# Kernel optimization log

Measured on AMD Instinct MI355X. Metric: run time of the kernel, lower is better.

The kernel has to match this reference:

```python
import jax, jax.numpy as jnp
import numpy as np

N_NODES = 100000
N_EDGES = 3200000
D = 256


def setup_inputs() -> dict:
    key = jax.random.key(0)
    ks = jax.random.split(key, 8)
    ego_embeddings = jax.random.normal(ks[0], (N_NODES, D), dtype=jnp.float32) * 0.1
    edge_vals = jax.random.uniform(ks[1], (N_EDGES,), dtype=jnp.float32) / 32.0  # ~normalized adjacency
    W1 = jax.random.normal(ks[2], (D, D), dtype=jnp.float32) * (1.0 / np.sqrt(D))
    b1 = jnp.zeros((D,), dtype=jnp.float32)
    W2 = jax.random.normal(ks[3], (D, D), dtype=jnp.float32) * (1.0 / np.sqrt(D))
    b2 = jnp.zeros((D,), dtype=jnp.float32)
    edge_rows = jax.random.randint(ks[4], (N_EDGES,), 0, N_NODES, dtype=jnp.int32)
    edge_cols = jax.random.randint(ks[5], (N_EDGES,), 0, N_NODES, dtype=jnp.int32)
    return {"ego_embeddings": ego_embeddings, "edge_vals": edge_vals,
            "W1": W1, "b1": b1, "W2": W2, "b2": b2,
            "edge_rows": edge_rows, "edge_cols": edge_cols}


def reference(ego_embeddings, edge_vals, W1, b1, W2, b2, edge_rows, edge_cols):
    # SpMM: side = A_in @ ego  (A_in in COO: rows, cols, vals)
    n = ego_embeddings.shape[0]
    gathered = ego_embeddings[edge_cols] * edge_vals[:, None]      # [E, D]
    side = jax.ops.segment_sum(gathered, edge_rows, num_segments=n)  # [N, D]
    # bi-interaction aggregator
    sum_emb = jax.nn.leaky_relu((ego_embeddings + side) @ W1.T + b1, negative_slope=0.01)
    bi_emb = jax.nn.leaky_relu((ego_embeddings * side) @ W2.T + b2, negative_slope=0.01)
    # dropout p=0.0 -> identity
    return sum_emb + bi_emb
```

## Files before the change

### kernel.cpp

```cpp
#include <hip/hip_runtime.h>
#include <hip/hip_fp16.h>
#include <stdint.h>

#define D 256
#define CHSH 13

typedef __attribute__((ext_vector_type(8))) short short8;
typedef __attribute__((ext_vector_type(4))) float floatx4;

__device__ __forceinline__ ushort f2bf(float f) {
    union { float f; uint32_t u; } v; v.f = f;
    uint32_t u = v.u;
    u += 0x7fffu + ((u >> 16) & 1u);
    return (ushort)(u >> 16);
}
__device__ __forceinline__ float bf2f(ushort h) {
    union { uint32_t u; float f; } v; v.u = ((uint32_t)h) << 16;
    return v.f;
}


__global__ void k_hist(const int* __restrict__ er, const int* __restrict__ ec,
                       int* __restrict__ bp, int E, int NCH) {
    int e = blockIdx.x * 256 + threadIdx.x;
    if (e >= E) return;
    atomicAdd(&bp[er[e] * NCH + (ec[e] >> CHSH)], 1);
}

__global__ void k_red(const int* __restrict__ bp, int* __restrict__ part, int nb) {
    __shared__ int s[256];
    int t = threadIdx.x;
    int base = blockIdx.x * 1024 + t * 4;
    int v = 0;
#pragma unroll
    for (int j = 0; j < 4; ++j) if (base + j < nb) v += bp[base + j];
    s[t] = v; __syncthreads();
    for (int off = 128; off; off >>= 1) {
        if (t < off) s[t] += s[t + off];
        __syncthreads();
    }
    if (t == 0) part[blockIdx.x] = s[0];
}

__global__ __launch_bounds__(1024) void k_scanpart(int* __restrict__ part, int np) {
    __shared__ int s[1024];
    int t = threadIdx.x;
    int p0 = (2 * t < np) ? part[2 * t] : 0;
    int p1 = (2 * t + 1 < np) ? part[2 * t + 1] : 0;
    int v = p0 + p1;
    s[t] = v; __syncthreads();
    for (int off = 1; off < 1024; off <<= 1) {
        int x = (t >= off) ? s[t - off] : 0;
        __syncthreads();
        s[t] += x;
        __syncthreads();
    }
    int excl = s[t] - v;
    if (2 * t < np) part[2 * t] = excl;
    if (2 * t + 1 < np) part[2 * t + 1] = excl + p0;
}

__global__ void k_scan3(int* __restrict__ bp, const int* __restrict__ part, int nb) {
    __shared__ int s[256];
    int t = threadIdx.x;
    int base = blockIdx.x * 1024 + t * 4;
    int d0 = 0, d1 = 0, d2 = 0, d3 = 0;
    if (base     < nb) d0 = bp[base];
    if (base + 1 < nb) d1 = bp[base + 1];
    if (base + 2 < nb) d2 = bp[base + 2];
    if (base + 3 < nb) d3 = bp[base + 3];
    int sum = d0 + d1 + d2 + d3;
    s[t] = sum; __syncthreads();
    for (int off = 1; off < 256; off <<= 1) {
        int x = (t >= off) ? s[t - off] : 0;
        __syncthreads();
        s[t] += x;
        __syncthreads();
    }
    int run = part[blockIdx.x] + s[t] - sum;
    if (base     < nb) bp[base]     = run; run += d0;
    if (base + 1 < nb) bp[base + 1] = run; run += d1;
    if (base + 2 < nb) bp[base + 2] = run; run += d2;
    if (base + 3 < nb) bp[base + 3] = run;
}

__global__ void k_scatter(const int* __restrict__ er, const int* __restrict__ ec,
                          const float* __restrict__ ev, int* __restrict__ bp,
                          uint32_t* __restrict__ csr, int E, int NCH) {
    int e = blockIdx.x * 256 + threadIdx.x;
    if (e >= E) return;
    int col = ec[e];
    int p = atomicAdd(&bp[er[e] * NCH + (col >> CHSH)], 1);
    ushort hb = __half_as_ushort(__float2half_rn(ev[e]));
    csr[p] = ((uint32_t)col << 15) | (uint32_t)hb;
}

__global__ void k_cvt(const float4* __restrict__ ego, ushort4* __restrict__ ego_bf,
                      const float4* __restrict__ W1, const float4* __restrict__ W2,
                      ushort4* __restrict__ W1b, ushort4* __restrict__ W2b, int n4) {
    int i = blockIdx.x * 256 + threadIdx.x;
    const float4* src;
    ushort4* dst;
    if (i < n4) { src = ego + i; dst = ego_bf + i; }
    else {
        int j = i - n4;
        if (j >= 32768) return;
        int k = j & 16383;
        src = ((j < 16384) ? W1 : W2) + k;
        dst = ((j < 16384) ? W1b : W2b) + k;
    }
    float4 f = *src;
    ushort4 u;
    u.x = f2bf(f.x); u.y = f2bf(f.y); u.z = f2bf(f.z); u.w = f2bf(f.w);
    *dst = u;
}

__global__ void k_spmm(const ushort* __restrict__ ego_bf, const int* __restrict__ bp,
                       const uint32_t* __restrict__ csr,
                       ushort* __restrict__ X1, ushort* __restrict__ X2, int n, int NCH) {
    int gtid = blockIdx.x * 256 + threadIdx.x;
    int node = gtid >> 6;
    int lane = gtid & 63;
    if (node >= n) return;
    int beg = (node == 0) ? 0 : bp[node * NCH - 1];
    int end = bp[(node + 1) * NCH - 1];
    int d0 = lane * 4;
    float a0 = 0.f, a1 = 0.f, a2 = 0.f, a3 = 0.f;
    int e = beg;
    for (; e + 8 <= end; e += 8) {
        uint32_t w[8];
#pragma unroll
        for (int j = 0; j < 8; ++j) w[j] = csr[e + j];
        ushort4 u[8];
#pragma unroll
        for (int j = 0; j < 8; ++j)
            u[j] = *(const ushort4*)(ego_bf + (size_t)(w[j] >> 15) * D + d0);
#pragma unroll
        for (int j = 0; j < 8; ++j) {
            float v = __half2float(__ushort_as_half((ushort)(w[j] & 0x7fff)));
            a0 += v * bf2f(u[j].x);
            a1 += v * bf2f(u[j].y);
            a2 += v * bf2f(u[j].z);
            a3 += v * bf2f(u[j].w);
        }
    }
    for (; e < end; ++e) {
        uint32_t w = csr[e];
        float v = __half2float(__ushort_as_half((ushort)(w & 0x7fff)));
        ushort4 u = *(const ushort4*)(ego_bf + (size_t)(w >> 15) * D + d0);
        a0 += v * bf2f(u.x);
        a1 += v * bf2f(u.y);
        a2 += v * bf2f(u.z);
        a3 += v * bf2f(u.w);
    }
    ushort4 eg = *(const ushort4*)(ego_bf + (size_t)node * D + d0);
    float e0 = bf2f(eg.x), e1 = bf2f(eg.y), e2 = bf2f(eg.z), e3 = bf2f(eg.w);
    ushort4 o1, o2;
    o1.x = f2bf(e0 + a0); o2.x = f2bf(e0 * a0);
    o1.y = f2bf(e1 + a1); o2.y = f2bf(e1 * a1);
    o1.z = f2bf(e2 + a2); o2.z = f2bf(e2 * a2);
    o1.w = f2bf(e3 + a3); o2.w = f2bf(e3 * a3);
    *(ushort4*)(X1 + (size_t)node * D + d0) = o1;
    *(ushort4*)(X2 + (size_t)node * D + d0) = o2;
}

__global__ __launch_bounds__(256) void k_gemm(
        const ushort* __restrict__ X1, const ushort* __restrict__ X2,
        const ushort* __restrict__ W1b, const ushort* __restrict__ W2b,
        const float* __restrict__ b1, const float* __restrict__ b2,
        float* __restrict__ out, int n) {
    int lane = threadIdx.x & 63;
    int w = threadIdx.x >> 6;
    int l16 = lane & 15, quad = lane >> 4;
    int row0 = blockIdx.x * 64;
    int colw = w * 64;

    floatx4 acc1[4][4], acc2[4][4];
#pragma unroll
    for (int i = 0; i < 4; ++i)
#pragma unroll
        for (int j = 0; j < 4; ++j) { acc1[i][j] = (floatx4)0.f; acc2[i][j] = (floatx4)0.f; }

    for (int kk = 0; kk < D; kk += 32) {
        short8 a[4], b[4];
#pragma unroll
        for (int mt = 0; mt < 4; ++mt)
            a[mt] = *(const short8*)(X1 + (size_t)(row0 + mt * 16 + l16) * D + kk + quad * 8);
#pragma unroll
        for (int nt = 0; nt < 4; ++nt)
            b[nt] = *(const short8*)(W1b + (size_t)(colw + nt * 16 + l16) * D + kk + quad * 8);
#pragma unroll
        for (int mt = 0; mt < 4; ++mt)
#pragma unroll
            for (int nt = 0; nt < 4; ++nt)
                acc1[mt][nt] = __builtin_amdgcn_mfma_f32_16x16x32_bf16(a[mt], b[nt], acc1[mt][nt], 0, 0, 0);
    }
    for (int kk = 0; kk < D; kk += 32) {
        short8 a[4], b[4];
#pragma unroll
        for (int mt = 0; mt < 4; ++mt)
            a[mt] = *(const short8*)(X2 + (size_t)(row0 + mt * 16 + l16) * D + kk + quad * 8);
#pragma unroll
        for (int nt = 0; nt < 4; ++nt)
            b[nt] = *(const short8*)(W2b + (size_t)(colw + nt * 16 + l16) * D + kk + quad * 8);
#pragma unroll
        for (int mt = 0; mt < 4; ++mt)
#pragma unroll
            for (int nt = 0; nt < 4; ++nt)
                acc2[mt][nt] = __builtin_amdgcn_mfma_f32_16x16x32_bf16(a[mt], b[nt], acc2[mt][nt], 0, 0, 0);
    }

#pragma unroll
    for (int nt = 0; nt < 4; ++nt) {
        int col = colw + nt * 16 + l16;
        float bb1 = b1[col], bb2 = b2[col];
#pragma unroll
        for (int mt = 0; mt < 4; ++mt) {
            int row = row0 + mt * 16 + quad * 4;
#pragma unroll
            for (int r = 0; r < 4; ++r) {
                if (row + r < n) {
                    float v1 = acc1[mt][nt][r] + bb1;
                    v1 = v1 > 0.f ? v1 : 0.01f * v1;
                    float v2 = acc2[mt][nt][r] + bb2;
                    v2 = v2 > 0.f ? v2 : 0.01f * v2;
                    out[(size_t)(row + r) * D + col] = v1 + v2;
                }
            }
        }
    }
}

extern "C" void kernel_launch(void* const* d_in, const int* in_sizes, int n_in,
                              void* d_out, int out_size, void* d_ws, size_t ws_size,
                              hipStream_t stream) {
    const float* ego   = (const float*)d_in[0];
    const float* evals = (const float*)d_in[1];
    const float* W1    = (const float*)d_in[2];
    const float* b1    = (const float*)d_in[3];
    const float* W2    = (const float*)d_in[4];
    const float* b2    = (const float*)d_in[5];
    const int* erows   = (const int*)d_in[6];
    const int* ecols   = (const int*)d_in[7];
    float* out = (float*)d_out;

    int n = in_sizes[0] / D;
    int E = in_sizes[1];
    int npad = (n + 63) & ~63;
    int NCH = (n + (1 << CHSH) - 1) >> CHSH;
    int nb = n * NCH;
    int np = (nb + 1023) / 1024;

    char* p = (char*)d_ws;
    auto alloc = [&](size_t bytes) {
        char* q = p;
        p += (bytes + 511) & ~(size_t)511;
        return q;
    };
    ushort* ego_bf = (ushort*)alloc((size_t)n * D * 2);
    ushort* X1     = (ushort*)alloc((size_t)npad * D * 2);
    ushort* X2     = (ushort*)alloc((size_t)npad * D * 2);
    ushort* W1b    = (ushort*)alloc((size_t)D * D * 2);
    ushort* W2b    = (ushort*)alloc((size_t)D * D * 2);
    int* bp        = (int*)alloc((size_t)nb * 4);
    int* part      = (int*)alloc((size_t)np * 4);
    uint32_t* csr  = (uint32_t*)alloc((size_t)E * 4);

    hipMemsetAsync(bp, 0, (size_t)nb * 4, stream);
    k_hist<<<(E + 255) / 256, 256, 0, stream>>>(erows, ecols, bp, E, NCH);
    k_red<<<np, 256, 0, stream>>>(bp, part, nb);
    k_scanpart<<<1, 1024, 0, stream>>>(part, np);
    k_scan3<<<np, 256, 0, stream>>>(bp, part, nb);
    k_scatter<<<(E + 255) / 256, 256, 0, stream>>>(erows, ecols, evals, bp, csr, E, NCH);

    int n4 = n * (D / 4);
    k_cvt<<<(n4 + 32768 + 255) / 256, 256, 0, stream>>>((const float4*)ego, (ushort4*)ego_bf,
                                                        (const float4*)W1, (const float4*)W2,
                                                        (ushort4*)W1b, (ushort4*)W2b, n4);

    k_spmm<<<(n * 64 + 255) / 256, 256, 0, stream>>>(ego_bf, bp, csr, X1, X2, n, NCH);

    k_gemm<<<npad / 64, 256, 0, stream>>>(X1, X2, W1b, W2b, b1, b2, out, n);
}
```

Baseline: 897.9 us.

## Precompute bucket+payload in histogram and partition scatter atomics by XCD range

The histogram pass now also computes each edge's bucket index and packed CSR payload, storing both as a 64-bit aux entry in the X1 buffer, which is free at that point. The scatter kernel launches 8x more blocks, each tagged by blockIdx&7. Each block reads aux but only handles edges whose bucket falls in its eighth of the bucket range, so atomics and csr writes for a given bp region stay in one XCD's L2. This trades 8x redundant reads of the 25.6MB aux array for better L2 locality of the atomics, and it assumes blocks are dispatched round-robin across XCDs.

```diff
diff --git a/kernel.cpp b/kernel.cpp
--- a/kernel.cpp
+++ b/kernel.cpp
@@ -21,10 +21,18 @@
 
 
 __global__ void k_hist(const int* __restrict__ er, const int* __restrict__ ec,
-                       int* __restrict__ bp, int E, int NCH) {
+                       const float* __restrict__ ev,
+                       int* __restrict__ bp, uint64_t* __restrict__ aux,
+                       int E, int NCH) {
     int e = blockIdx.x * 256 + threadIdx.x;
     if (e >= E) return;
-    atomicAdd(&bp[er[e] * NCH + (ec[e] >> CHSH)], 1);
+    int row = er[e];
+    int col = ec[e];
+    int b = row * NCH + (col >> CHSH);
+    atomicAdd(&bp[b], 1);
+    ushort hb = __half_as_ushort(__float2half_rn(ev[e]));
+    uint32_t payload = ((uint32_t)col << 15) | (uint32_t)hb;
+    aux[e] = ((uint64_t)(uint32_t)b << 32) | payload;
 }
 
 __global__ void k_red(const int* __restrict__ bp, int* __restrict__ part, int nb) {
@@ -84,15 +92,19 @@
     if (base + 3 < nb) bp[base + 3] = run;
 }
 
-__global__ void k_scatter(const int* __restrict__ er, const int* __restrict__ ec,
-                          const float* __restrict__ ev, int* __restrict__ bp,
-                          uint32_t* __restrict__ csr, int E, int NCH) {
-    int e = blockIdx.x * 256 + threadIdx.x;
+__global__ void k_scatter(const uint64_t* __restrict__ aux,
+                          int* __restrict__ bp, uint32_t* __restrict__ csr,
+                          int E, int BW) {
+    int xcd = blockIdx.x & 7;
+    int j = blockIdx.x >> 3;
+    int e = j * 256 + threadIdx.x;
     if (e >= E) return;
-    int col = ec[e];
-    int p = atomicAdd(&bp[er[e] * NCH + (col >> CHSH)], 1);
-    ushort hb = __half_as_ushort(__float2half_rn(ev[e]));
-    csr[p] = ((uint32_t)col << 15) | (uint32_t)hb;
+    uint64_t a = aux[e];
+    int b = (int)(a >> 32);
+    int lo = xcd * BW;
+    if (b < lo || b >= lo + BW) return;
+    int p = atomicAdd(&bp[b], 1);
+    csr[p] = (uint32_t)a;
 }
 
 __global__ void k_cvt(const float4* __restrict__ ego, ushort4* __restrict__ ego_bf,
@@ -250,6 +262,7 @@
     int NCH = (n + (1 << CHSH) - 1) >> CHSH;
     int nb = n * NCH;
     int np = (nb + 1023) / 1024;
+    int BW = (nb + 7) / 8;
 
     char* p = (char*)d_ws;
     auto alloc = [&](size_t bytes) {
@@ -266,12 +279,15 @@
     int* part      = (int*)alloc((size_t)np * 4);
     uint32_t* csr  = (uint32_t*)alloc((size_t)E * 4);
 
+    uint64_t* aux = (uint64_t*)X1;
+
     hipMemsetAsync(bp, 0, (size_t)nb * 4, stream);
-    k_hist<<<(E + 255) / 256, 256, 0, stream>>>(erows, ecols, bp, E, NCH);
+    int EB = (E + 255) / 256;
+    k_hist<<<EB, 256, 0, stream>>>(erows, ecols, evals, bp, aux, E, NCH);
     k_red<<<np, 256, 0, stream>>>(bp, part, nb);
     k_scanpart<<<1, 1024, 0, stream>>>(part, np);
     k_scan3<<<np, 256, 0, stream>>>(bp, part, nb);
-    k_scatter<<<(E + 255) / 256, 256, 0, stream>>>(erows, ecols, evals, bp, csr, E, NCH);
+    k_scatter<<<8 * EB, 256, 0, stream>>>(aux, bp, csr, E, BW);
 
     int n4 = n * (D / 4);
     k_cvt<<<(n4 + 32768 + 255) / 256, 256, 0, stream>>>((const float4*)ego, (ushort4*)ego_bf,
```

After: 833.3 us. -7.2%, faster.
